# Performance work log

Measured on AMD Instinct MI355X. Metric: run time of the kernel, lower is better.

Reference implementation:

```python
import jax, jax.numpy as jnp
import numpy as np
from jax import lax

EPS = 1e-5

def _instance_norm(x):
    # per-sample, per-channel over HW, affine=False (torch default), biased var
    m = jnp.mean(x, axis=(2, 3), keepdims=True)
    v = jnp.mean((x - m) ** 2, axis=(2, 3), keepdims=True)
    return (x - m) / jnp.sqrt(v + EPS)

def _lrelu(x):
    return jax.nn.leaky_relu(x, 0.2)

def _conv(x, w, b, stride=1, pad=0):
    y = lax.conv_general_dilated(x, w, (stride, stride), ((pad, pad), (pad, pad)),
                                 dimension_numbers=('NCHW', 'OIHW', 'NCHW'))
    return y + b[None, :, None, None]

def _conv_transpose(x, w, b):
    # torch ConvTranspose2d(k=3, stride=2, padding=1, output_padding=1)
    # == dilated conv with lhs_dilation=2, pad (k-1-p, k-1-p+op) = (1, 2),
    # kernel spatially flipped and in/out swapped. w: (Cin, Cout, 3, 3)
    wt = jnp.flip(w, axis=(2, 3)).transpose(1, 0, 2, 3)  # (Cout, Cin, 3, 3)
    y = lax.conv_general_dilated(x, wt, (1, 1), ((1, 2), (1, 2)),
                                 lhs_dilation=(2, 2),
                                 dimension_numbers=('NCHW', 'OIHW', 'NCHW'))
    return y + b[None, :, None, None]

def _reflect_pad1(x):
    return jnp.pad(x, ((0, 0), (0, 0), (1, 1), (1, 1)), mode='reflect')

def _nearest_resize(x, out_h, out_w):
    in_h, in_w = x.shape[2], x.shape[3]
    iy = (jnp.arange(out_h) * (in_h / out_h)).astype(jnp.int32)
    ix = (jnp.arange(out_w) * (in_w / out_w)).astype(jnp.int32)
    return x[:, :, iy][:, :, :, ix]

def setup_inputs() -> dict:
    key = jax.random.key(0)
    ks = jax.random.split(key, 12)
    B, S, H, W = 8, 19, 256, 256
    out_nc = 512
    inp = jax.random.normal(ks[0], (B, 3, H, W), dtype=jnp.float32)
    labels = jax.random.randint(ks[1], (B, 1, H, W), 0, S)
    segmap = (labels == jnp.arange(S).reshape(1, S, 1, 1)).astype(jnp.float32)
    sc = 0.05
    return {
        'input': inp, 'segmap': segmap,
        'w1': jax.random.normal(ks[2], (32, 3, 3, 3), jnp.float32) * sc,
        'b1': jnp.zeros((32,), jnp.float32),
        'w2': jax.random.normal(ks[3], (64, 32, 3, 3), jnp.float32) * sc,
        'b2': jnp.zeros((64,), jnp.float32),
        'w3': jax.random.normal(ks[4], (128, 64, 3, 3), jnp.float32) * sc,
        'b3': jnp.zeros((128,), jnp.float32),
        'w4': jax.random.normal(ks[5], (128, 256, 3, 3), jnp.float32) * sc,  # torch convT layout (Cin, Cout, kh, kw)
        'b4': jnp.zeros((256,), jnp.float32),
        'w5': jax.random.normal(ks[6], (out_nc, 256, 3, 3), jnp.float32) * sc,
        'b5': jnp.zeros((out_nc,), jnp.float32),
    }

def _backbone(x, w1, b1, w2, b2, w3, b3, w4, b4, w5, b5):
    x = _lrelu(_instance_norm(_conv(_reflect_pad1(x), w1, b1)))          # [B,32,256,256]
    x = _lrelu(_instance_norm(_conv(x, w2, b2, stride=2, pad=1)))        # [B,64,128,128]
    x = _lrelu(_instance_norm(_conv(x, w3, b3, stride=2, pad=1)))        # [B,128,64,64]
    x = _lrelu(_instance_norm(_conv_transpose(x, w4, b4)))               # [B,256,128,128]
    x = jnp.tanh(_conv(_reflect_pad1(x), w5, b5))                        # [B,512,128,128]
    return x

def reference(input, segmap, w1, b1, w2, b2, w3, b3, w4, b4, w5, b5):
    codes = _backbone(input, w1, b1, w2, b2, w3, b3, w4, b4, w5, b5)
    seg = _nearest_resize(segmap, codes.shape[2], codes.shape[3])
    mask = (seg > 0).astype(codes.dtype)                                  # segmap.bool()
    sums = jnp.einsum('bchw,bshw->bsc', codes, mask)                      # masked sum per (b, class)
    counts = jnp.sum(mask, axis=(2, 3))[:, :, None]                       # [B,S,1]
    return jnp.where(counts > 0, sums / jnp.maximum(counts, 1.0), 0.0)    # [B,S,C]
```

## Files before the change

### kernel.cpp

```cpp
#include <hip/hip_runtime.h>

#define LB __launch_bounds__(256)

constexpr int S = 19;

typedef __attribute__((ext_vector_type(8))) short frag16;
typedef __attribute__((ext_vector_type(8))) ushort ushort8;
typedef __attribute__((ext_vector_type(4))) float f32x4;

__device__ __forceinline__ int reflect256(int i) { return i < 0 ? -i : (i > 255 ? 510 - i : i); }
__device__ __forceinline__ int reflect128(int i) { return i < 0 ? -i : (i > 127 ? 254 - i : i); }

__device__ __forceinline__ ushort f2bf(float f) {
    union { float f; uint u; } a; a.f = f;
    uint r = a.u + 0x7fffu + ((a.u >> 16) & 1u);
    return (ushort)(r >> 16);
}
__device__ __forceinline__ float bf2f(ushort u) {
    union { uint u; float f; } a; a.u = ((uint)u) << 16; return a.f;
}

__global__ LB void k_conv1cl(const float* __restrict__ in, const float* __restrict__ w,
                             const float* __restrict__ bias, ushort* __restrict__ out) {
    __shared__ float Wr[864];
    __shared__ float Bs[32];
    int t = threadIdx.x;
    for (int e = t; e < 864; e += 256) Wr[e] = w[e];
    if (t < 32) Bs[t] = bias[t];
    __syncthreads();
    int idx = blockIdx.x * 256 + t;
    int x = idx & 255, y = (idx >> 8) & 255, b = idx >> 16;
    float v[27];
    #pragma unroll
    for (int ci = 0; ci < 3; ++ci) {
        const float* ip = in + ((b * 3 + ci) << 16);
        #pragma unroll
        for (int ky = 0; ky < 3; ++ky) {
            int iy = reflect256(y + ky - 1);
            #pragma unroll
            for (int kx = 0; kx < 3; ++kx) {
                int ix = reflect256(x + kx - 1);
                v[ci * 9 + ky * 3 + kx] = ip[(iy << 8) + ix];
            }
        }
    }
    ushort* op = out + (long)idx * 32;
    #pragma unroll
    for (int g = 0; g < 4; ++g) {
        ushort8 o;
        #pragma unroll
        for (int j = 0; j < 8; ++j) {
            int co = g * 8 + j;
            float a = Bs[co];
            #pragma unroll
            for (int k = 0; k < 27; ++k) a += v[k] * Wr[co * 27 + k];
            o[j] = f2bf(a);
        }
        *(ushort8*)(op + g * 8) = o;
    }
}

template <int C, int PB, int SPLITS>
__global__ LB void k_stats_cl(const ushort* __restrict__ x,
                              float* __restrict__ psum, float* __restrict__ pss) {
    __shared__ float lsum[C], lss[C];
    int b = blockIdx.x / SPLITS, sp = blockIdx.x % SPLITS;
    int t = threadIdx.x;
    if (t < C) { lsum[t] = 0.f; lss[t] = 0.f; }
    __syncthreads();
    constexpr int CG = C / 8;
    constexpr int PO = 256 / CG;
    int c0 = (t % CG) * 8;
    int po = t / CG;
    float s[8], ss[8];
    #pragma unroll
    for (int k = 0; k < 8; ++k) { s[k] = 0.f; ss[k] = 0.f; }
    const ushort* base = x + ((long)b * SPLITS + sp) * (long)PB * C;
    for (int p = po; p < PB; p += PO) {
        ushort8 v = *(const ushort8*)(base + (long)p * C + c0);
        #pragma unroll
        for (int k = 0; k < 8; ++k) {
            float f = bf2f(v[k]);
            s[k] += f; ss[k] += f * f;
        }
    }
    #pragma unroll
    for (int k = 0; k < 8; ++k) {
        atomicAdd(&lsum[c0 + k], s[k]);
        atomicAdd(&lss[c0 + k], ss[k]);
    }
    __syncthreads();
    if (t < C) {
        psum[blockIdx.x * C + t] = lsum[t];
        pss[blockIdx.x * C + t] = lss[t];
    }
}

template <int C, int SPLITS, int P>
__global__ LB void k_red_cl(const float* __restrict__ psum, const float* __restrict__ pss,
                            float* __restrict__ mean, float* __restrict__ istd) {
    int idx = blockIdx.x * 256 + threadIdx.x;
    if (idx >= 8 * C) return;
    int b = idx / C, c = idx % C;
    float s = 0.f, ss = 0.f;
    for (int sp = 0; sp < SPLITS; ++sp) {
        s += psum[(b * SPLITS + sp) * C + c];
        ss += pss[(b * SPLITS + sp) * C + c];
    }
    float m = s / (float)P;
    float v = ss / (float)P - m * m;
    mean[idx] = m;
    istd[idx] = rsqrtf(v + 1e-5f);
}

template <int C, int P>
__global__ LB void k_nl_cl(ushort* __restrict__ x, const float* __restrict__ mean,
                           const float* __restrict__ istd) {
    long e = ((long)blockIdx.x * 256 + threadIdx.x) * 8;
    int c0 = (int)(e % C);
    int b = (int)(e / ((long)P * C));
    ushort8 v = *(ushort8*)(x + e);
    const float* mp = mean + b * C + c0;
    const float* ip = istd + b * C + c0;
    #pragma unroll
    for (int k = 0; k < 8; ++k) {
        float u = (bf2f(v[k]) - mp[k]) * ip[k];
        u = u > 0.f ? u : 0.2f * u;
        v[k] = f2bf(u);
    }
    *(ushort8*)(x + e) = v;
}

__global__ LB void k_wtall(const float* __restrict__ w2, const float* __restrict__ w3,
                           const float* __restrict__ w4, const float* __restrict__ w5,
                           ushort* __restrict__ t2, ushort* __restrict__ t3,
                           ushort* __restrict__ t4, ushort* __restrict__ t5) {
    int e = blockIdx.x * 256 + threadIdx.x;
    if (e < 18432) {
        int ci = e & 31, co = (e >> 5) & 63, tap = e >> 11;
        t2[e] = f2bf(w2[(co * 32 + ci) * 9 + tap]);
    } else if (e < 18432 + 73728) {
        int e2 = e - 18432;
        int ci = e2 & 63, co = (e2 >> 6) & 127, tap = e2 >> 13;
        t3[e2] = f2bf(w3[(co * 64 + ci) * 9 + tap]);
    } else if (e < 18432 + 73728 + 294912) {
        int e3 = e - (18432 + 73728);
        int ci = e3 & 127, co = (e3 >> 7) & 255, tap = e3 >> 15;
        t4[e3] = f2bf(w4[ci * 2304 + co * 9 + tap]);
    } else {
        int e4 = e - (18432 + 73728 + 294912);
        int ci = e4 & 255, co = (e4 >> 8) & 511, tap = e4 >> 17;
        t5[e4] = f2bf(w5[(co * 256 + ci) * 9 + tap]);
    }
}

__global__ LB void k_conv2m(const ushort* __restrict__ xin, const ushort* __restrict__ wt,
                            const float* __restrict__ bias, ushort* __restrict__ xout) {
    int bx = blockIdx.x;
    int y = bx & 127, b = bx >> 7;
    int t = threadIdx.x, w = t >> 6, lane = t & 63;
    int col0 = w * 32;
    int lanep = lane & 15, hi = lane >> 4;

    f32x4 acc[4][2];
    #pragma unroll
    for (int m = 0; m < 4; ++m)
        #pragma unroll
        for (int n = 0; n < 2; ++n) acc[m][n] = (f32x4){0.f, 0.f, 0.f, 0.f};

    #pragma unroll
    for (int ky = 0; ky < 3; ++ky) {
        int iy = 2 * y + ky - 1;
        if (iy < 0) continue;
        #pragma unroll
        for (int kx = 0; kx < 3; ++kx) {
            int tap = ky * 3 + kx;
            const ushort* wb = wt + ((tap * 64 + lanep) << 5) + hi * 8;
            frag16 av[4];
            #pragma unroll
            for (int m = 0; m < 4; ++m) av[m] = *(const frag16*)(wb + ((m * 16) << 5));
            frag16 bv[2];
            #pragma unroll
            for (int n = 0; n < 2; ++n) {
                int xo = col0 + n * 16 + lanep;
                int ix = 2 * xo + kx - 1;
                frag16 vv = (frag16)(short)0;
                if (ix >= 0)
                    vv = *(const frag16*)(xin + ((((long)(b * 256 + iy)) << 8) + ix) * 32 + hi * 8);
                bv[n] = vv;
            }
            #pragma unroll
            for (int m = 0; m < 4; ++m)
                #pragma unroll
                for (int n = 0; n < 2; ++n)
                    acc[m][n] = __builtin_amdgcn_mfma_f32_16x16x32_bf16(av[m], bv[n], acc[m][n], 0, 0, 0);
        }
    }
    float bvv[4][4];
    #pragma unroll
    for (int m = 0; m < 4; ++m)
        #pragma unroll
        for (int r = 0; r < 4; ++r) bvv[m][r] = bias[m * 16 + hi * 4 + r];
    #pragma unroll
    for (int n = 0; n < 2; ++n) {
        int xo = col0 + n * 16 + lanep;
        long pb = ((((long)(b * 128 + y)) << 7) + xo) * 64 + hi * 4;
        #pragma unroll
        for (int m = 0; m < 4; ++m) {
            ushort4 o;
            o.x = f2bf(acc[m][n][0] + bvv[m][0]);
            o.y = f2bf(acc[m][n][1] + bvv[m][1]);
            o.z = f2bf(acc[m][n][2] + bvv[m][2]);
            o.w = f2bf(acc[m][n][3] + bvv[m][3]);
            *(ushort4*)(xout + pb + m * 16) = o;
        }
    }
}

__global__ LB void k_conv3m(const ushort* __restrict__ xin, const ushort* __restrict__ wt,
                            const float* __restrict__ bias, ushort* __restrict__ xout) {
    int bx = blockIdx.x;
    int y = bx & 63, b = bx >> 6;
    int t = threadIdx.x, w = t >> 6, lane = t & 63;
    int co0 = (w >> 1) * 64;
    int col0 = (w & 1) * 32;
    int lanep = lane & 15, hi = lane >> 4;

    f32x4 acc[4][2];
    #pragma unroll
    for (int m = 0; m < 4; ++m)
        #pragma unroll
        for (int n = 0; n < 2; ++n) acc[m][n] = (f32x4){0.f, 0.f, 0.f, 0.f};

    #pragma unroll
    for (int ky = 0; ky < 3; ++ky) {
        int iy = 2 * y + ky - 1;
        if (iy < 0) continue;
        #pragma unroll
        for (int kx = 0; kx < 3; ++kx) {
            int tap = ky * 3 + kx;
            #pragma unroll
            for (int ck = 0; ck < 2; ++ck) {
                int ci0 = ck * 32;
                const ushort* wb = wt + ((tap * 128 + co0 + lanep) << 6) + ci0 + hi * 8;
                frag16 av[4];
                #pragma unroll
                for (int m = 0; m < 4; ++m) av[m] = *(const frag16*)(wb + ((m * 16) << 6));
                frag16 bv[2];
                #pragma unroll
                for (int n = 0; n < 2; ++n) {
                    int xo = col0 + n * 16 + lanep;
                    int ix = 2 * xo + kx - 1;
                    frag16 vv = (frag16)(short)0;
                    if (ix >= 0)
                        vv = *(const frag16*)(xin + ((((long)(b * 128 + iy)) << 7) + ix) * 64 + ci0 + hi * 8);
                    bv[n] = vv;
                }
                #pragma unroll
                for (int m = 0; m < 4; ++m)
                    #pragma unroll
                    for (int n = 0; n < 2; ++n)
                        acc[m][n] = __builtin_amdgcn_mfma_f32_16x16x32_bf16(av[m], bv[n], acc[m][n], 0, 0, 0);
            }
        }
    }
    float bvv[4][4];
    #pragma unroll
    for (int m = 0; m < 4; ++m)
        #pragma unroll
        for (int r = 0; r < 4; ++r) bvv[m][r] = bias[co0 + m * 16 + hi * 4 + r];
    #pragma unroll
    for (int n = 0; n < 2; ++n) {
        int xo = col0 + n * 16 + lanep;
        long pb = ((((long)(b * 64 + y)) << 6) + xo) * 128 + co0 + hi * 4;
        #pragma unroll
        for (int m = 0; m < 4; ++m) {
            ushort4 o;
            o.x = f2bf(acc[m][n][0] + bvv[m][0]);
            o.y = f2bf(acc[m][n][1] + bvv[m][1]);
            o.z = f2bf(acc[m][n][2] + bvv[m][2]);
            o.w = f2bf(acc[m][n][3] + bvv[m][3]);
            *(ushort4*)(xout + pb + m * 16) = o;
        }
    }
}

__global__ LB void k_convt4m(const ushort* __restrict__ x3l, const ushort* __restrict__ wt,
                             const float* __restrict__ bias, ushort* __restrict__ xl) {
    int bx = blockIdx.x;
    int parity = bx & 3;
    int py = parity >> 1, px = parity & 1;
    int rg = (bx >> 2) & 15;
    int ct = (bx >> 6) & 3;
    int b  = bx >> 8;
    int co0 = ct * 64;
    int t = threadIdx.x;
    int w = t >> 6;
    int ip = rg * 4 + w;
    int lane = t & 63;
    int lanep = lane & 15;
    int hi = lane >> 4;
    int laneq = hi * 8;

    f32x4 acc[4][4];
    #pragma unroll
    for (int m = 0; m < 4; ++m)
        #pragma unroll
        for (int n = 0; n < 4; ++n) acc[m][n] = (f32x4){0.f, 0.f, 0.f, 0.f};

    #pragma unroll
    for (int ky = 0; ky < 3; ++ky) {
        if (((ky + py) & 1) == 0) continue;
        int i = ip + ((py == 1 && ky == 0) ? 1 : 0);
        if (i >= 64) continue;
        #pragma unroll
        for (int kx = 0; kx < 3; ++kx) {
            if (((kx + px) & 1) == 0) continue;
            int dxp = (px == 1 && kx == 0) ? 1 : 0;
            int tap = ky * 3 + kx;
            const ushort* wbase = wt + (((long)tap * 256 + co0 + lanep) << 7) + laneq;
            const ushort* xbase = x3l + ((((long)b << 12) + (i << 6)) << 7) + laneq;
            #pragma unroll
            for (int ci0 = 0; ci0 < 128; ci0 += 32) {
                frag16 av[4], bv[4];
                #pragma unroll
                for (int m = 0; m < 4; ++m)
                    av[m] = *(const frag16*)(wbase + ((m * 16) << 7) + ci0);
                #pragma unroll
                for (int n = 0; n < 4; ++n) {
                    int j = n * 16 + lanep + dxp;
                    bool valid = j < 64;
                    frag16 v = *(const frag16*)(xbase + ((valid ? j : 63) << 7) + ci0);
                    if (!valid) v = (frag16)(short)0;
                    bv[n] = v;
                }
                #pragma unroll
                for (int m = 0; m < 4; ++m)
                    #pragma unroll
                    for (int n = 0; n < 4; ++n)
                        acc[m][n] = __builtin_amdgcn_mfma_f32_16x16x32_bf16(av[m], bv[n], acc[m][n], 0, 0, 0);
            }
        }
    }

    float bvv[4][4];
    #pragma unroll
    for (int m = 0; m < 4; ++m)
        #pragma unroll
        for (int r = 0; r < 4; ++r)
            bvv[m][r] = bias[co0 + m * 16 + hi * 4 + r];
    int y = 2 * ip + py;
    #pragma unroll
    for (int n = 0; n < 4; ++n) {
        int x = 2 * (n * 16 + lanep) + px;
        long pb = ((((long)b << 14) + (y << 7) + x) << 8) + co0 + hi * 4;
        #pragma unroll
        for (int m = 0; m < 4; ++m) {
            ushort4 o;
            o.x = f2bf(acc[m][n][0] + bvv[m][0]);
            o.y = f2bf(acc[m][n][1] + bvv[m][1]);
            o.z = f2bf(acc[m][n][2] + bvv[m][2]);
            o.w = f2bf(acc[m][n][3] + bvv[m][3]);
            *(ushort4*)(xl + pb + m * 16) = o;
        }
    }
}

__global__ LB void k_label(const float* __restrict__ segmap, int* __restrict__ lab,
                           int* __restrict__ counts) {
    __shared__ int h[S];
    if (threadIdx.x < S) h[threadIdx.x] = 0;
    __syncthreads();
    int idx = blockIdx.x * 256 + threadIdx.x;
    int x = idx & 127, y = (idx >> 7) & 127, b = idx >> 14;
    const float* sp = segmap + (long)b * S * 65536 + (y << 1) * 256 + (x << 1);
    int s = 0;
    for (int c = 0; c < S; ++c) {
        if (sp[c * 65536] > 0.f) { s = c; break; }
    }
    lab[idx] = s;
    atomicAdd(&h[s], 1);
    __syncthreads();
    if (threadIdx.x < S) atomicAdd(&counts[b * S + threadIdx.x], h[threadIdx.x]);
}

__global__ void __launch_bounds__(256, 2)
k_conv5m(const ushort* __restrict__ xl, const ushort* __restrict__ wt,
         const float* __restrict__ bias, const int* __restrict__ lab,
         float* __restrict__ sumbuf) {
    __shared__ __align__(16) ushort Xs[2080 * 8];
    __shared__ __align__(16) ushort Ws[2304 * 8];
    float* part = (float*)Xs;

    int bx = blockIdx.x;
    int yp = bx & 63;
    int ct = (bx >> 6) & 7;
    int b  = bx >> 9;
    int y0 = yp * 2, cob = ct * 64;
    int t = threadIdx.x;
    int w = t >> 6;
    int lane = t & 63;
    int row_w = w & 1;
    int col0 = (w >> 1) * 64;
    int lanep = lane & 15;
    int hi = lane >> 4;
    int xw8 = (hi ^ ((lanep >> 1) & 3)) * 8;

    long xbase = (long)b << 14;
    int xg[9], xo[9];
    #pragma unroll
    for (int k = 0; k < 9; ++k) {
        int e = t + k * 256;
        if (e < 2080) {
            int q = e & 3, p = e >> 2;
            int r = p / 130, c = p - r * 130;
            int gy = reflect128(y0 - 1 + r);
            int gc = reflect128(c - 1);
            xg[k] = (int)(((xbase + (gy << 7) + gc) << 8) + q * 8);
            xo[k] = (p * 4 + (q ^ ((p >> 1) & 3))) * 8;
        } else { xg[k] = 0; xo[k] = 0; }
    }
    int wg[9], wo[9];
    #pragma unroll
    for (int k = 0; k < 9; ++k) {
        int e = t + k * 256;
        int q = e & 3, p = e >> 2;
        wg[k] = (((p >> 6) * 512 + cob + (p & 63)) << 8) + q * 8;
        wo[k] = (p * 4 + (q ^ ((p >> 1) & 3))) * 8;
    }
    bool xtail = (t < 32);

    f32x4 acc[4][4];
    #pragma unroll
    for (int m = 0; m < 4; ++m)
        #pragma unroll
        for (int n = 0; n < 4; ++n) acc[m][n] = (f32x4){0.f, 0.f, 0.f, 0.f};

    frag16 gx_[9], gw_[9];

    #pragma unroll
    for (int k = 0; k < 8; ++k) gx_[k] = *(const frag16*)(xl + xg[k]);
    if (xtail) gx_[8] = *(const frag16*)(xl + xg[8]);
    #pragma unroll
    for (int k = 0; k < 9; ++k) gw_[k] = *(const frag16*)(wt + wg[k]);
    #pragma unroll
    for (int k = 0; k < 8; ++k) *(frag16*)(Xs + xo[k]) = gx_[k];
    if (xtail) *(frag16*)(Xs + xo[8]) = gx_[8];
    #pragma unroll
    for (int k = 0; k < 9; ++k) *(frag16*)(Ws + wo[k]) = gw_[k];
    __syncthreads();

    #pragma unroll 1
    for (int c8 = 0; c8 < 8; ++c8) {
        int cin = c8 * 32 + 32;
        if (c8 < 7) {
            #pragma unroll
            for (int k = 0; k < 8; ++k) gx_[k] = *(const frag16*)(xl + xg[k] + cin);
            if (xtail) gx_[8] = *(const frag16*)(xl + xg[8] + cin);
            #pragma unroll
            for (int k = 0; k < 9; ++k) gw_[k] = *(const frag16*)(wt + wg[k] + cin);
        }
        #pragma unroll
        for (int tap = 0; tap < 9; ++tap) {
            int ky = tap / 3, kx = tap % 3;
            frag16 av[4];
            #pragma unroll
            for (int m = 0; m < 4; ++m)
                av[m] = *(const frag16*)(Ws + (tap * 64 + m * 16 + lanep) * 32 + xw8);
            int p0 = (row_w + ky) * 130 + col0 + kx + lanep;
            int bo = p0 * 32 + (hi ^ ((p0 >> 1) & 3)) * 8;
            frag16 bf[4];
            #pragma unroll
            for (int n = 0; n < 4; ++n)
                bf[n] = *(const frag16*)(Xs + bo + n * 512);
            #pragma unroll
            for (int m = 0; m < 4; ++m)
                #pragma unroll
                for (int n = 0; n < 4; ++n)
                    acc[m][n] = __builtin_amdgcn_mfma_f32_16x16x32_bf16(av[m], bf[n], acc[m][n], 0, 0, 0);
        }
        __syncthreads();
        if (c8 < 7) {
            #pragma unroll
            for (int k = 0; k < 8; ++k) *(frag16*)(Xs + xo[k]) = gx_[k];
            if (xtail) *(frag16*)(Xs + xo[8]) = gx_[8];
            #pragma unroll
            for (int k = 0; k < 9; ++k) *(frag16*)(Ws + wo[k]) = gw_[k];
        }
        __syncthreads();
    }

    float bv[4][4];
    #pragma unroll
    for (int m = 0; m < 4; ++m)
        #pragma unroll
        for (int r = 0; r < 4; ++r)
            bv[m][r] = bias[cob + m * 16 + hi * 4 + r];

    for (int e = t; e < S * 64; e += 256) part[e] = 0.f;
    __syncthreads();

    int y = y0 + row_w;
    #pragma unroll
    for (int n = 0; n < 4; ++n) {
        int x = col0 + n * 16 + lanep;
        int s = lab[(b << 14) + (y << 7) + x];
        #pragma unroll
        for (int m = 0; m < 4; ++m)
            #pragma unroll
            for (int r = 0; r < 4; ++r)
                atomicAdd(&part[s * 64 + m * 16 + hi * 4 + r], tanhf(acc[m][n][r] + bv[m][r]));
    }
    __syncthreads();
    for (int e = t; e < S * 64; e += 256) {
        int s = e >> 6, col = e & 63;
        atomicAdd(&sumbuf[((b * S + s) << 9) + cob + col], part[e]);
    }
}

__global__ LB void k_final(const float* __restrict__ sumbuf, const int* __restrict__ counts,
                           float* __restrict__ out) {
    int idx = blockIdx.x * 256 + threadIdx.x;
    int tt = idx >> 9;
    int s = tt % S, b = tt / S;
    int cnt = counts[b * S + s];
    out[idx] = cnt > 0 ? sumbuf[idx] / (float)cnt : 0.f;
}

extern "C" void kernel_launch(void* const* d_in, const int* in_sizes, int n_in,
                              void* d_out, int out_size, void* d_ws, size_t ws_size,
                              hipStream_t stream) {
    const float* input  = (const float*)d_in[0];
    const float* segmap = (const float*)d_in[1];
    const float* w1 = (const float*)d_in[2];  const float* b1 = (const float*)d_in[3];
    const float* w2 = (const float*)d_in[4];  const float* b2 = (const float*)d_in[5];
    const float* w3 = (const float*)d_in[6];  const float* b3 = (const float*)d_in[7];
    const float* w4 = (const float*)d_in[8];  const float* b4 = (const float*)d_in[9];
    const float* w5 = (const float*)d_in[10]; const float* b5 = (const float*)d_in[11];
    float* out = (float*)d_out;

    float* ws = (float*)d_ws;
    ushort* xl    = (ushort*)ws;
    ushort* x1l   = (ushort*)(ws + 16777216);
    ushort* x2l   = (ushort*)(ws + 25165824);
    ushort* x3l   = (ushort*)(ws + 29360128);
    float* sumbuf = ws + 31457280;
    float* mean   = ws + 31535104;
    float* istd   = ws + 31537152;
    int*   lab    = (int*)(ws + 31539200);
    int*   counts = (int*)(ws + 31670272);
    ushort* wt5   = (ushort*)(ws + 31670528);
    ushort* wt4t  = (ushort*)(ws + 32260352);
    ushort* wt2   = (ushort*)(ws + 32407808);
    ushort* wt3   = (ushort*)(ws + 32417024);
    float* psum   = ws + 32453888;
    float* pss    = ws + 32519424;

    hipMemsetAsync(sumbuf, 0, 77824 * sizeof(float), stream);
    hipMemsetAsync(counts, 0, 256 * sizeof(int), stream);

    k_wtall<<<6120, 256, 0, stream>>>(w2, w3, w4, w5, wt2, wt3, wt4t, wt5);
    k_conv1cl<<<2048, 256, 0, stream>>>(input, w1, b1, x1l);
    k_stats_cl<32, 1024, 64><<<512, 256, 0, stream>>>(x1l, psum, pss);
    k_red_cl<32, 64, 65536><<<1, 256, 0, stream>>>(psum, pss, mean, istd);
    k_nl_cl<32, 65536><<<8192, 256, 0, stream>>>(x1l, mean, istd);
    k_conv2m<<<1024, 256, 0, stream>>>(x1l, wt2, b2, x2l);
    k_stats_cl<64, 512, 32><<<256, 256, 0, stream>>>(x2l, psum, pss);
    k_red_cl<64, 32, 16384><<<2, 256, 0, stream>>>(psum, pss, mean, istd);
    k_nl_cl<64, 16384><<<4096, 256, 0, stream>>>(x2l, mean, istd);
    k_conv3m<<<512, 256, 0, stream>>>(x2l, wt3, b3, x3l);
    k_stats_cl<128, 256, 16><<<128, 256, 0, stream>>>(x3l, psum, pss);
    k_red_cl<128, 16, 4096><<<4, 256, 0, stream>>>(psum, pss, mean, istd);
    k_nl_cl<128, 4096><<<2048, 256, 0, stream>>>(x3l, mean, istd);
    k_convt4m<<<2048, 256, 0, stream>>>(x3l, wt4t, b4, xl);
    k_stats_cl<256, 512, 32><<<256, 256, 0, stream>>>(xl, psum, pss);
    k_red_cl<256, 32, 16384><<<8, 256, 0, stream>>>(psum, pss, mean, istd);
    k_nl_cl<256, 16384><<<16384, 256, 0, stream>>>(xl, mean, istd);
    k_label<<<512, 256, 0, stream>>>(segmap, lab, counts);
    k_conv5m<<<4096, 256, 0, stream>>>(xl, wt5, b5, lab, sumbuf);
    k_final<<<304, 256, 0, stream>>>(sumbuf, counts, out);
}
```

Baseline: 927.0 us.

## Load conv5 weight fragments directly from global into registers, dropping LDS staging

The conv5 MFMA kernel no longer stages weight tiles in shared memory. Each wave loads its A fragments straight from global memory, prefetching the next tap's fragments one step ahead of use. This removes the weight LDS buffer and its writes and reads, which halves shared-memory use and may raise occupancy. In exchange, the two waves that share the same output channels each fetch the same weights from global/L2, and every fetch is exposed latency that only a single tap of compute covers.

```diff
diff --git a/kernel.cpp b/kernel.cpp
--- a/kernel.cpp
+++ b/kernel.cpp
@@ -389,7 +389,6 @@
          const float* __restrict__ bias, const int* __restrict__ lab,
          float* __restrict__ sumbuf) {
     __shared__ __align__(16) ushort Xs[2080 * 8];
-    __shared__ __align__(16) ushort Ws[2304 * 8];
     float* part = (float*)Xs;
 
     int bx = blockIdx.x;
@@ -404,7 +403,7 @@
     int col0 = (w >> 1) * 64;
     int lanep = lane & 15;
     int hi = lane >> 4;
-    int xw8 = (hi ^ ((lanep >> 1) & 3)) * 8;
+    int laneq = hi * 8;
 
     long xbase = (long)b << 14;
     int xg[9], xo[9];
@@ -420,53 +419,52 @@
             xo[k] = (p * 4 + (q ^ ((p >> 1) & 3))) * 8;
         } else { xg[k] = 0; xo[k] = 0; }
     }
-    int wg[9], wo[9];
-    #pragma unroll
-    for (int k = 0; k < 9; ++k) {
-        int e = t + k * 256;
-        int q = e & 3, p = e >> 2;
-        wg[k] = (((p >> 6) * 512 + cob + (p & 63)) << 8) + q * 8;
-        wo[k] = (p * 4 + (q ^ ((p >> 1) & 3))) * 8;
-    }
     bool xtail = (t < 32);
 
+    int wbo[4];
+    #pragma unroll
+    for (int m = 0; m < 4; ++m)
+        wbo[m] = ((cob + m * 16 + lanep) << 8) + laneq;
+
     f32x4 acc[4][4];
     #pragma unroll
     for (int m = 0; m < 4; ++m)
         #pragma unroll
         for (int n = 0; n < 4; ++n) acc[m][n] = (f32x4){0.f, 0.f, 0.f, 0.f};
 
-    frag16 gx_[9], gw_[9];
+    frag16 gx_[9];
+    frag16 a_cur[4];
+
+    #define LOADA(dst, tap, ci0)                                                   \
+        _Pragma("unroll")                                                          \
+        for (int m = 0; m < 4; ++m)                                                \
+            dst[m] = *(const frag16*)(wt + (tap) * 131072 + wbo[m] + (ci0));
 
     #pragma unroll
     for (int k = 0; k < 8; ++k) gx_[k] = *(const frag16*)(xl + xg[k]);
     if (xtail) gx_[8] = *(const frag16*)(xl + xg[8]);
-    #pragma unroll
-    for (int k = 0; k < 9; ++k) gw_[k] = *(const frag16*)(wt + wg[k]);
+    LOADA(a_cur, 0, 0);
     #pragma unroll
     for (int k = 0; k < 8; ++k) *(frag16*)(Xs + xo[k]) = gx_[k];
     if (xtail) *(frag16*)(Xs + xo[8]) = gx_[8];
-    #pragma unroll
-    for (int k = 0; k < 9; ++k) *(frag16*)(Ws + wo[k]) = gw_[k];
     __syncthreads();
 
     #pragma unroll 1
     for (int c8 = 0; c8 < 8; ++c8) {
-        int cin = c8 * 32 + 32;
+        int ci0 = c8 * 32;
         if (c8 < 7) {
             #pragma unroll
-            for (int k = 0; k < 8; ++k) gx_[k] = *(const frag16*)(xl + xg[k] + cin);
-            if (xtail) gx_[8] = *(const frag16*)(xl + xg[8] + cin);
-            #pragma unroll
-            for (int k = 0; k < 9; ++k) gw_[k] = *(const frag16*)(wt + wg[k] + cin);
+            for (int k = 0; k < 8; ++k) gx_[k] = *(const frag16*)(xl + xg[k] + ci0 + 32);
+            if (xtail) gx_[8] = *(const frag16*)(xl + xg[8] + ci0 + 32);
         }
         #pragma unroll
         for (int tap = 0; tap < 9; ++tap) {
             int ky = tap / 3, kx = tap % 3;
-            frag16 av[4];
-            #pragma unroll
-            for (int m = 0; m < 4; ++m)
-                av[m] = *(const frag16*)(Ws + (tap * 64 + m * 16 + lanep) * 32 + xw8);
+            frag16 a_use[4];
+            #pragma unroll
+            for (int m = 0; m < 4; ++m) a_use[m] = a_cur[m];
+            if (tap < 8) { LOADA(a_cur, tap + 1, ci0); }
+            else if (c8 < 7) { LOADA(a_cur, 0, ci0 + 32); }
             int p0 = (row_w + ky) * 130 + col0 + kx + lanep;
             int bo = p0 * 32 + (hi ^ ((p0 >> 1) & 3)) * 8;
             frag16 bf[4];
@@ -477,18 +475,17 @@
             for (int m = 0; m < 4; ++m)
                 #pragma unroll
                 for (int n = 0; n < 4; ++n)
-                    acc[m][n] = __builtin_amdgcn_mfma_f32_16x16x32_bf16(av[m], bf[n], acc[m][n], 0, 0, 0);
+                    acc[m][n] = __builtin_amdgcn_mfma_f32_16x16x32_bf16(a_use[m], bf[n], acc[m][n], 0, 0, 0);
         }
         __syncthreads();
         if (c8 < 7) {
             #pragma unroll
             for (int k = 0; k < 8; ++k) *(frag16*)(Xs + xo[k]) = gx_[k];
             if (xtail) *(frag16*)(Xs + xo[8]) = gx_[8];
-            #pragma unroll
-            for (int k = 0; k < 9; ++k) *(frag16*)(Ws + wo[k]) = gw_[k];
         }
         __syncthreads();
     }
+    #undef LOADA
 
     float bv[4][4];
     #pragma unroll
```

New measurement: 1.230 ms. +32.7%, slower.

## Double-buffer conv5 LDS tiles with direct global-to-LDS loads

Applied to the files above, without the earlier changes.

Replaces the register-staged global loads followed by LDS stores in the conv5 MFMA kernel with global_load_lds direct transfers into ping-pong LDS buffers. The swizzle moves from the LDS destination to the global source offset, so the lane-linear LDS write pattern still matches the existing reads. One barrier per channel chunk is removed and the prefetch registers (18 frag16) are freed, lowering register pressure and overlapping loads with MFMA. LDS use grows to about 140 KB per block, which with launch bounds of 2 blocks per CU may exceed the per-CU LDS capacity and cut occupancy to one block.

```diff
diff --git a/kernel.cpp b/kernel.cpp
--- a/kernel.cpp
+++ b/kernel.cpp
@@ -18,6 +18,12 @@
 }
 __device__ __forceinline__ float bf2f(ushort u) {
     union { uint u; float f; } a; a.u = ((uint)u) << 16; return a.f;
+}
+
+__device__ __forceinline__ void gll16(const void* g, void* l) {
+    __builtin_amdgcn_global_load_lds(
+        (const __attribute__((address_space(1))) void*)g,
+        (__attribute__((address_space(3))) void*)l, 16, 0, 0);
 }
 
 __global__ LB void k_conv1cl(const float* __restrict__ in, const float* __restrict__ w,
@@ -388,9 +394,9 @@
 k_conv5m(const ushort* __restrict__ xl, const ushort* __restrict__ wt,
          const float* __restrict__ bias, const int* __restrict__ lab,
          float* __restrict__ sumbuf) {
-    __shared__ __align__(16) ushort Xs[2080 * 8];
-    __shared__ __align__(16) ushort Ws[2304 * 8];
-    float* part = (float*)Xs;
+    __shared__ __align__(16) ushort L[70144];
+    float* part = (float*)L;
+    constexpr int XS0 = 0, XS1 = 16640, WS0 = 33280, WS1 = 51712;
 
     int bx = blockIdx.x;
     int yp = bx & 63;
@@ -407,28 +413,20 @@
     int xw8 = (hi ^ ((lanep >> 1) & 3)) * 8;
 
     long xbase = (long)b << 14;
-    int xg[9], xo[9];
+    long xg[9]; int wg[9];
     #pragma unroll
     for (int k = 0; k < 9; ++k) {
         int e = t + k * 256;
+        int q = e & 3, p = e >> 2;
+        int qp = q ^ ((p >> 1) & 3);
         if (e < 2080) {
-            int q = e & 3, p = e >> 2;
             int r = p / 130, c = p - r * 130;
             int gy = reflect128(y0 - 1 + r);
             int gc = reflect128(c - 1);
-            xg[k] = (int)(((xbase + (gy << 7) + gc) << 8) + q * 8);
-            xo[k] = (p * 4 + (q ^ ((p >> 1) & 3))) * 8;
-        } else { xg[k] = 0; xo[k] = 0; }
-    }
-    int wg[9], wo[9];
-    #pragma unroll
-    for (int k = 0; k < 9; ++k) {
-        int e = t + k * 256;
-        int q = e & 3, p = e >> 2;
-        wg[k] = (((p >> 6) * 512 + cob + (p & 63)) << 8) + q * 8;
-        wo[k] = (p * 4 + (q ^ ((p >> 1) & 3))) * 8;
-    }
-    bool xtail = (t < 32);
+            xg[k] = ((xbase + (gy << 7) + gc) << 8) + qp * 8;
+        } else xg[k] = xbase << 8;
+        wg[k] = (((p >> 6) * 512 + cob + (p & 63)) << 8) + qp * 8;
+    }
 
     f32x4 acc[4][4];
     #pragma unroll
@@ -436,29 +434,26 @@
         #pragma unroll
         for (int n = 0; n < 4; ++n) acc[m][n] = (f32x4){0.f, 0.f, 0.f, 0.f};
 
-    frag16 gx_[9], gw_[9];
-
-    #pragma unroll
-    for (int k = 0; k < 8; ++k) gx_[k] = *(const frag16*)(xl + xg[k]);
-    if (xtail) gx_[8] = *(const frag16*)(xl + xg[8]);
-    #pragma unroll
-    for (int k = 0; k < 9; ++k) gw_[k] = *(const frag16*)(wt + wg[k]);
-    #pragma unroll
-    for (int k = 0; k < 8; ++k) *(frag16*)(Xs + xo[k]) = gx_[k];
-    if (xtail) *(frag16*)(Xs + xo[8]) = gx_[8];
-    #pragma unroll
-    for (int k = 0; k < 9; ++k) *(frag16*)(Ws + wo[k]) = gw_[k];
+    #pragma unroll
+    for (int k = 0; k < 8; ++k) gll16(xl + xg[k], L + XS0 + ((k << 8) + t) * 8);
+    if (t < 32) gll16(xl + xg[8], L + XS0 + ((8 << 8) + t) * 8);
+    #pragma unroll
+    for (int k = 0; k < 9; ++k) gll16(wt + wg[k], L + WS0 + ((k << 8) + t) * 8);
     __syncthreads();
 
     #pragma unroll 1
     for (int c8 = 0; c8 < 8; ++c8) {
-        int cin = c8 * 32 + 32;
+        const ushort* xs  = L + ((c8 & 1) ? XS1 : XS0);
+        const ushort* wsb = L + ((c8 & 1) ? WS1 : WS0);
         if (c8 < 7) {
-            #pragma unroll
-            for (int k = 0; k < 8; ++k) gx_[k] = *(const frag16*)(xl + xg[k] + cin);
-            if (xtail) gx_[8] = *(const frag16*)(xl + xg[8] + cin);
-            #pragma unroll
-            for (int k = 0; k < 9; ++k) gw_[k] = *(const frag16*)(wt + wg[k] + cin);
+            int cin = (c8 + 1) * 32;
+            int xd = (c8 & 1) ? XS0 : XS1;
+            int wd = (c8 & 1) ? WS0 : WS1;
+            #pragma unroll
+            for (int k = 0; k < 8; ++k) gll16(xl + xg[k] + cin, L + xd + ((k << 8) + t) * 8);
+            if (t < 32) gll16(xl + xg[8] + cin, L + xd + ((8 << 8) + t) * 8);
+            #pragma unroll
+            for (int k = 0; k < 9; ++k) gll16(wt + wg[k] + cin, L + wd + ((k << 8) + t) * 8);
         }
         #pragma unroll
         for (int tap = 0; tap < 9; ++tap) {
@@ -466,26 +461,18 @@
             frag16 av[4];
             #pragma unroll
             for (int m = 0; m < 4; ++m)
-                av[m] = *(const frag16*)(Ws + (tap * 64 + m * 16 + lanep) * 32 + xw8);
+                av[m] = *(const frag16*)(wsb + (tap * 64 + m * 16 + lanep) * 32 + xw8);
             int p0 = (row_w + ky) * 130 + col0 + kx + lanep;
             int bo = p0 * 32 + (hi ^ ((p0 >> 1) & 3)) * 8;
             frag16 bf[4];
             #pragma unroll
             for (int n = 0; n < 4; ++n)
-                bf[n] = *(const frag16*)(Xs + bo + n * 512);
+                bf[n] = *(const frag16*)(xs + bo + n * 512);
             #pragma unroll
             for (int m = 0; m < 4; ++m)
                 #pragma unroll
                 for (int n = 0; n < 4; ++n)
                     acc[m][n] = __builtin_amdgcn_mfma_f32_16x16x32_bf16(av[m], bf[n], acc[m][n], 0, 0, 0);
-        }
-        __syncthreads();
-        if (c8 < 7) {
-            #pragma unroll
-            for (int k = 0; k < 8; ++k) *(frag16*)(Xs + xo[k]) = gx_[k];
-            if (xtail) *(frag16*)(Xs + xo[8]) = gx_[8];
-            #pragma unroll
-            for (int k = 0; k < 9; ++k) *(frag16*)(Ws + wo[k]) = gw_[k];
         }
         __syncthreads();
     }
```

Measured after the change: 1.013 ms. 9.2% more time.
